# Kernel optimization log

Measured on AMD Instinct MI355X. Metric: run time of the kernel, lower is better.

## Reference

```python
import jax, jax.numpy as jnp
import numpy as np

SEQ_LEN, BATCH, VOCAB, EMB, HID, LAYERS = 70, 64, 10000, 512, 512, 2


def setup_inputs() -> dict:
    key = jax.random.key(0)
    ks = jax.random.split(key, 6)
    u = lambda k, shape: jax.random.uniform(k, shape, jnp.float32, -0.1, 0.1)
    return {
        "inputs": jax.random.randint(ks[0], (SEQ_LEN, BATCH), 0, VOCAB),  # token ids
        "hidden": jnp.zeros((LAYERS, BATCH, HID), jnp.float32),           # init_hidden()
        "emb_table": jax.random.normal(ks[1], (VOCAB, EMB), jnp.float32),  # nn.Embedding default N(0,1)
        "W0": u(ks[2], (HID, EMB + HID)),
        "b0": jnp.zeros((HID,), jnp.float32),
        "W1": u(ks[3], (HID, 2 * HID)),
        "b1": jnp.zeros((HID,), jnp.float32),
        "Wout": u(ks[4], (VOCAB, HID)),
        "bout": jnp.zeros((VOCAB,), jnp.float32),
    }


def reference(inputs, hidden, emb_table, W0, b0, W1, b1, Wout, bout):
    # Embedding lookup for whole sequence: (T, B, E)
    emb = emb_table[inputs]
    Ws, bs = [W0, W1], [b0, b1]

    def step(h, x_t):  # h: (L, B, H), x_t: (B, E)
        inp = x_t
        new_h = []
        for l in range(LAYERS):  # small fixed depth; layers are structurally distinct
            cat = jnp.concatenate([inp, h[l]], axis=1)          # (B, E+H) or (B, 2H)
            out = jnp.tanh(cat @ Ws[l].T + bs[l])               # (B, H)
            new_h.append(out)
            inp = out
        logits_t = jnp.tanh(inp @ Wout.T + bout)                # (B, V) (original applies Tanh to logits)
        return jnp.stack(new_h), logits_t

    h_final, logits = jax.lax.scan(step, hidden, emb)
    return logits, h_final
```

## Files before the change

### kernel.cpp

```cpp
#include <hip/hip_runtime.h>

#define T 70
#define B 64
#define E 512
#define H 512
#define V 10000
#define NP 10112
#define TB (T*B)
#define SLOT (H*B)
#define LOGITS_N (T*B*V)

#define WV_F 81920
#define WL_F 36864
#define WS_F4 35840
#define WLAYER 262144

typedef __attribute__((ext_vector_type(8))) short bh8;
typedef __attribute__((ext_vector_type(4))) float f32x4;

__device__ __forceinline__ float ftanh(float x) {
    float e = __expf(2.0f * x);
    return 1.0f - 2.0f / (e + 1.0f);
}

__device__ __forceinline__ unsigned short f2bf(float x) {
    unsigned int u = __float_as_uint(x);
    u += 0x7FFFu + ((u >> 16) & 1u);
    return (unsigned short)(u >> 16);
}
__device__ __forceinline__ float bf2f(unsigned short h) {
    return __uint_as_float(((unsigned int)h) << 16);
}

__global__ __launch_bounds__(256) void gather_emb(const int* __restrict__ ids,
                                                  const float* __restrict__ emb,
                                                  float* __restrict__ X) {
    int i = blockIdx.x * 256 + threadIdx.x;
    if (i >= TB * (E / 4)) return;
    int tok = i >> 7;
    int e4 = i & 127;
    int id = ids[tok];
    ((float4*)X)[i] = ((const float4*)emb)[id * 128 + e4];
}

__global__ __launch_bounds__(256) void pack_w(const float* __restrict__ W0,
                                              const float* __restrict__ W1,
                                              float* __restrict__ Wpk) {
    int g = blockIdx.x * 256 + threadIdx.x;
    int l = g >= 93184;
    int u = g - l * 93184;
    const float* S = l ? W1 : W0;
    float* D = Wpk + l * WLAYER;

    if (u < 20480) {
        int n2 = u & 255, q = u >> 8;
        int j2 = q % 40, hq = q / 40;
        int k = hq * 256 + 2 * j2;
        int n0 = 2 * n2;
        float2 r0 = *(const float2*)(S + (size_t)n0 * 1024 + 512 + k);
        float2 r1 = *(const float2*)(S + (size_t)(n0 + 1) * 1024 + 512 + k);
        ((float4*)D)[(hq * 40 + j2) * 256 + n2] = make_float4(r0.x, r1.x, r0.y, r1.y);
    } else if (u < 20480 + WS_F4) {
        int v = u - 20480;
        int n2 = v & 255, q = v >> 8;
        int j2s = q % 70, hq = q / 70;
        int k = hq * 256 + 116 + 2 * j2s;
        int n0 = 2 * n2;
        float2 r0 = *(const float2*)(S + (size_t)n0 * 1024 + 512 + k);
        float2 r1 = *(const float2*)(S + (size_t)(n0 + 1) * 1024 + 512 + k);
        ((float4*)D)[(WV_F + WL_F) / 4 + (hq * 70 + j2s) * 256 + n2] =
            make_float4(r0.x, r1.x, r0.y, r1.y);
    } else {
        int w = u - (20480 + WS_F4);
        int n = w & 511, q = w >> 9;
        int jr = q % 36, hq = q / 36;
        int k = hq * 256 + 80 + jr;
        D[WV_F + (hq * 36 + jr) * 512 + n] = S[(size_t)n * 1024 + 512 + k];
    }
}

__global__ __launch_bounds__(256) void split_w(const float* __restrict__ Wout,
                                               unsigned short* __restrict__ Whi,
                                               unsigned short* __restrict__ Wlo) {
    int i = blockIdx.x * 256 + threadIdx.x;
    if (i >= NP * 512) return;
    int v = i >> 9;
    float x = (v < V) ? Wout[i] : 0.f;
    unsigned short hi = f2bf(x);
    Whi[i] = hi;
    Wlo[i] = f2bf(x - bf2f(hi));
}

__global__ __launch_bounds__(256) void gemm_p0(const float* __restrict__ X,
                                               const float* __restrict__ W0,
                                               const float* __restrict__ b0v,
                                               float* __restrict__ P0) {
    __shared__ float As[32][68];
    __shared__ float Ws[32][68];
    int t = blockIdx.y;
    int n0 = blockIdx.x * 64;
    int tid = threadIdx.x;
    int bq = tid & 15;
    int nq = tid >> 4;
    const float* A = X + t * 64 * E;
    float acc[4][4] = {{0.f}};

    for (int kc = 0; kc < 512; kc += 32) {
        for (int i = tid; i < 512; i += 256) {
            int bb = i >> 3, kq = i & 7;
            float4 a = *(const float4*)(A + bb * E + kc + kq * 4);
            As[kq*4+0][bb] = a.x; As[kq*4+1][bb] = a.y;
            As[kq*4+2][bb] = a.z; As[kq*4+3][bb] = a.w;
        }
        for (int i = tid; i < 512; i += 256) {
            int nn = i >> 3, kq = i & 7;
            float4 w = *(const float4*)(W0 + (size_t)(n0 + nn) * 1024 + kc + kq * 4);
            Ws[kq*4+0][nn] = w.x; Ws[kq*4+1][nn] = w.y;
            Ws[kq*4+2][nn] = w.z; Ws[kq*4+3][nn] = w.w;
        }
        __syncthreads();
#pragma unroll
        for (int kk = 0; kk < 32; kk++) {
            float4 a = *(const float4*)&As[kk][bq * 4];
            float4 w = *(const float4*)&Ws[kk][nq * 4];
            acc[0][0] += a.x*w.x; acc[0][1] += a.x*w.y; acc[0][2] += a.x*w.z; acc[0][3] += a.x*w.w;
            acc[1][0] += a.y*w.x; acc[1][1] += a.y*w.y; acc[1][2] += a.y*w.z; acc[1][3] += a.y*w.w;
            acc[2][0] += a.z*w.x; acc[2][1] += a.z*w.y; acc[2][2] += a.z*w.z; acc[2][3] += a.z*w.w;
            acc[3][0] += a.w*w.x; acc[3][1] += a.w*w.y; acc[3][2] += a.w*w.z; acc[3][3] += a.w*w.w;
        }
        __syncthreads();
    }
    int nb = n0 + nq * 4;
    float4 bo = *(const float4*)(b0v + nb);
#pragma unroll
    for (int i = 0; i < 4; i++) {
        int bb = bq * 4 + i;
        float4 r = make_float4(acc[i][0] + bo.x, acc[i][1] + bo.y,
                               acc[i][2] + bo.z, acc[i][3] + bo.w);
        *(float4*)(P0 + (size_t)t * SLOT + bb * 512 + nb) = r;
    }
}

__global__ __launch_bounds__(256) void gemm_p1(const float* __restrict__ H0,
                                               const float* __restrict__ W1,
                                               const float* __restrict__ b1v,
                                               float* __restrict__ P1) {
    __shared__ float As[32][68];
    __shared__ float Ws[32][68];
    int t = blockIdx.y;
    int n0 = blockIdx.x * 64;
    int tid = threadIdx.x;
    int bq = tid & 15;
    int nq = tid >> 4;
    const float* A = H0 + (size_t)t * SLOT;
    float acc[4][4] = {{0.f}};

    for (int kc = 0; kc < 512; kc += 32) {
        for (int i = tid; i < 512; i += 256) {
            int bb = i >> 3, kq = i & 7;
            float4 a = *(const float4*)(A + bb * 512 + kc + kq * 4);
            As[kq*4+0][bb] = a.x; As[kq*4+1][bb] = a.y;
            As[kq*4+2][bb] = a.z; As[kq*4+3][bb] = a.w;
        }
        for (int i = tid; i < 512; i += 256) {
            int nn = i >> 3, kq = i & 7;
            float4 w = *(const float4*)(W1 + (size_t)(n0 + nn) * 1024 + kc + kq * 4);
            Ws[kq*4+0][nn] = w.x; Ws[kq*4+1][nn] = w.y;
            Ws[kq*4+2][nn] = w.z; Ws[kq*4+3][nn] = w.w;
        }
        __syncthreads();
#pragma unroll
        for (int kk = 0; kk < 32; kk++) {
            float4 a = *(const float4*)&As[kk][bq * 4];
            float4 w = *(const float4*)&Ws[kk][nq * 4];
            acc[0][0] += a.x*w.x; acc[0][1] += a.x*w.y; acc[0][2] += a.x*w.z; acc[0][3] += a.x*w.w;
            acc[1][0] += a.y*w.x; acc[1][1] += a.y*w.y; acc[1][2] += a.y*w.z; acc[1][3] += a.y*w.w;
            acc[2][0] += a.z*w.x; acc[2][1] += a.z*w.y; acc[2][2] += a.z*w.z; acc[2][3] += a.z*w.w;
            acc[3][0] += a.w*w.x; acc[3][1] += a.w*w.y; acc[3][2] += a.w*w.z; acc[3][3] += a.w*w.w;
        }
        __syncthreads();
    }
    int nb = n0 + nq * 4;
    float4 bo = *(const float4*)(b1v + nb);
#pragma unroll
    for (int i = 0; i < 4; i++) {
        int bb = bq * 4 + i;
        float4 r = make_float4(acc[i][0] + bo.x, acc[i][1] + bo.y,
                               acc[i][2] + bo.z, acc[i][3] + bo.w);
        *(float4*)(P1 + (size_t)t * SLOT + bb * 512 + nb) = r;
    }
}

#define RPT40(X) X(0) X(1) X(2) X(3) X(4) X(5) X(6) X(7) X(8) X(9) X(10) X(11) \
  X(12) X(13) X(14) X(15) X(16) X(17) X(18) X(19) X(20) X(21) X(22) X(23) \
  X(24) X(25) X(26) X(27) X(28) X(29) X(30) X(31) X(32) X(33) X(34) X(35) \
  X(36) X(37) X(38) X(39)
#define RPT20P(X) X(0,0,1) X(1,2,3) X(2,4,5) X(3,6,7) X(4,8,9) X(5,10,11) \
  X(6,12,13) X(7,14,15) X(8,16,17) X(9,18,19) X(10,20,21) X(11,22,23) \
  X(12,24,25) X(13,26,27) X(14,28,29) X(15,30,31) X(16,32,33) X(17,34,35) \
  X(18,36,37) X(19,38,39)

__global__ __launch_bounds__(512, 2) void chain_hyb(const float* __restrict__ P,
                                                    const float* __restrict__ hidden,
                                                    const float* __restrict__ Wp,
                                                    float* __restrict__ Hist,
                                                    unsigned short* __restrict__ Hhi,
                                                    unsigned short* __restrict__ Hlo,
                                                    float* __restrict__ out,
                                                    int layer) {
    __shared__ float lds_w[WL_F];
    __shared__ float hs[512];
    __shared__ float2 part2[256];
    int tid = threadIdx.x;
    int b   = blockIdx.x;
    int n2  = tid & 255;
    int hq  = tid >> 8;
    int n0  = 2 * n2;

    const float4* wv = (const float4*)Wp + hq * (40 * 256) + n2;
#define DECLW(i) float4 w##i = wv[(i) * 256];
    RPT40(DECLW)
#undef DECLW

    {
        const float4* wl4 = (const float4*)(Wp + WV_F);
        float4* l4 = (float4*)lds_w;
        for (int i = tid; i < WL_F / 4; i += 512) l4[i] = wl4[i];
    }
    hs[tid & 511] = hidden[layer * SLOT + b * 512 + (tid & 511)];

#define PINW(i) asm volatile("" : "+v"(w##i.x), "+v"(w##i.y), "+v"(w##i.z), "+v"(w##i.w));
    RPT40(PINW)
#undef PINW
    __syncthreads();

    const float4* wsp = (const float4*)(Wp + WV_F + WL_F) + hq * (70 * 256) + n2;
    const float4* hs4 = (const float4*)hs;
    const float2* ldsw2 = (const float2*)lds_w;
    int hql4 = hq * 64;
    int ksb  = hq * 256 + 116;

    for (int s = 0; s < T; s++) {
        float2 pin = make_float2(0.f, 0.f);
        if (hq == 0)
            pin = *(const float2*)(P + (size_t)s * SLOT + b * 512 + n0);

        float ax = 0.f, ay = 0.f;

#pragma unroll 8
        for (int j = 0; j < 70; j++) {
            float4 wv4 = wsp[j * 256];
            float2 h2 = *(const float2*)&hs[ksb + 2 * j];
            ax += wv4.x * h2.x + wv4.z * h2.y;
            ay += wv4.y * h2.x + wv4.w * h2.y;
        }

#define FMAV(m, A, B2) { float4 h4 = hs4[hql4 + (m)]; \
        ax += w##A.x * h4.x + w##A.z * h4.y + w##B2.x * h4.z + w##B2.z * h4.w; \
        ay += w##A.y * h4.x + w##A.w * h4.y + w##B2.y * h4.z + w##B2.w * h4.w; }
        RPT20P(FMAV)
#undef FMAV

#pragma unroll
        for (int g = 0; g < 9; g++) {
            float4 h4 = hs4[hql4 + 20 + g];
            float2 l0 = ldsw2[(hq * 36 + 4 * g + 0) * 256 + n2];
            float2 l1 = ldsw2[(hq * 36 + 4 * g + 1) * 256 + n2];
            float2 l2 = ldsw2[(hq * 36 + 4 * g + 2) * 256 + n2];
            float2 l3 = ldsw2[(hq * 36 + 4 * g + 3) * 256 + n2];
            ax += l0.x * h4.x + l1.x * h4.y + l2.x * h4.z + l3.x * h4.w;
            ay += l0.y * h4.x + l1.y * h4.y + l2.y * h4.z + l3.y * h4.w;
        }

        if (hq) part2[n2] = make_float2(ax, ay);
        __syncthreads();
        if (hq == 0) {
            float2 pr = part2[n2];
            float o0 = ftanh(pin.x + ax + pr.x);
            float o1 = ftanh(pin.y + ay + pr.y);
            hs[n0] = o0; hs[n0 + 1] = o1;
            if (layer == 0) {
                *(float2*)(Hist + (size_t)s * SLOT + b * 512 + n0) = make_float2(o0, o1);
            } else {
                size_t m = (size_t)(s * 64 + b) * 512 + n0;
                unsigned short h0 = f2bf(o0), h1 = f2bf(o1);
                Hhi[m] = h0;     Hhi[m + 1] = h1;
                Hlo[m] = f2bf(o0 - bf2f(h0));
                Hlo[m + 1] = f2bf(o1 - bf2f(h1));
            }
        }
        __syncthreads();
    }

    out[LOGITS_N + layer * SLOT + b * 512 + tid] = hs[tid];
}

__global__ __launch_bounds__(256, 2) void logits_mfma(const unsigned short* __restrict__ Ahi,
                                                      const unsigned short* __restrict__ Alo,
                                                      const unsigned short* __restrict__ Whi,
                                                      const unsigned short* __restrict__ Wlo,
                                                      const float* __restrict__ boutv,
                                                      float* __restrict__ out) {
    __shared__ unsigned short Ah[128 * 40], Al[128 * 40];
    __shared__ unsigned short Bh[128 * 40], Bl[128 * 40];
    int tid = threadIdx.x;
    int v0 = blockIdx.x * 128;
    int mb = blockIdx.y * 128;
    int lane = tid & 63;
    int wid = tid >> 6;
    int lr = lane & 15;
    int lg = lane >> 4;
    int mhalf = (wid & 1) * 64;
    int nhalf = (wid >> 1) * 64;

    f32x4 acc[4][4];
#pragma unroll
    for (int i = 0; i < 4; i++)
#pragma unroll
        for (int j = 0; j < 4; j++) {
            acc[i][j][0] = 0.f; acc[i][j][1] = 0.f;
            acc[i][j][2] = 0.f; acc[i][j][3] = 0.f;
        }

    int aoff[4], boff[4];
#pragma unroll
    for (int f = 0; f < 4; f++) {
        aoff[f] = (mhalf + f * 16 + lr) * 40 + lg * 8;
        boff[f] = (nhalf + f * 16 + lr) * 40 + lg * 8;
    }

    for (int kb = 0; kb < 512; kb += 32) {
#pragma unroll
        for (int it = 0; it < 2; ++it) {
            int idx = it * 256 + tid;
            int r = idx >> 2, u = idx & 3;
            int d = r * 40 + u * 8;
            size_t sA = (size_t)(mb + r) * 512 + kb + u * 8;
            size_t sB = (size_t)(v0 + r) * 512 + kb + u * 8;
            *(uint4*)&Ah[d] = *(const uint4*)&Ahi[sA];
            *(uint4*)&Al[d] = *(const uint4*)&Alo[sA];
            *(uint4*)&Bh[d] = *(const uint4*)&Whi[sB];
            *(uint4*)&Bl[d] = *(const uint4*)&Wlo[sB];
        }
        __syncthreads();

        bh8 ah[4], al[4], bh[4], bl[4];
#pragma unroll
        for (int f = 0; f < 4; f++) {
            ah[f] = *(const bh8*)&Ah[aoff[f]];
            al[f] = *(const bh8*)&Al[aoff[f]];
            bh[f] = *(const bh8*)&Bh[boff[f]];
            bl[f] = *(const bh8*)&Bl[boff[f]];
        }
#pragma unroll
        for (int mf = 0; mf < 4; mf++)
#pragma unroll
            for (int nf = 0; nf < 4; nf++) {
                acc[mf][nf] = __builtin_amdgcn_mfma_f32_16x16x32_bf16(ah[mf], bh[nf], acc[mf][nf], 0, 0, 0);
                acc[mf][nf] = __builtin_amdgcn_mfma_f32_16x16x32_bf16(ah[mf], bl[nf], acc[mf][nf], 0, 0, 0);
                acc[mf][nf] = __builtin_amdgcn_mfma_f32_16x16x32_bf16(al[mf], bh[nf], acc[mf][nf], 0, 0, 0);
            }
        __syncthreads();
    }

#pragma unroll
    for (int nf = 0; nf < 4; nf++) {
        int v = v0 + nhalf + nf * 16 + lr;
        if (v < V) {
            float bo = boutv[v];
#pragma unroll
            for (int mf = 0; mf < 4; mf++) {
                int gm = mb + mhalf + mf * 16 + lg * 4;
#pragma unroll
                for (int reg = 0; reg < 4; reg++)
                    out[(size_t)(gm + reg) * V + v] = ftanh(acc[mf][nf][reg] + bo);
            }
        }
    }
}

extern "C" void kernel_launch(void* const* d_in, const int* in_sizes, int n_in,
                              void* d_out, int out_size, void* d_ws, size_t ws_size,
                              hipStream_t stream) {
    const int*   ids    = (const int*)d_in[0];
    const float* hidden = (const float*)d_in[1];
    const float* emb    = (const float*)d_in[2];
    const float* W0     = (const float*)d_in[3];
    const float* b0v    = (const float*)d_in[4];
    const float* W1     = (const float*)d_in[5];
    const float* b1v    = (const float*)d_in[6];
    const float* Wout   = (const float*)d_in[7];
    const float* boutv  = (const float*)d_in[8];
    float* out = (float*)d_out;
    float* ws  = (float*)d_ws;

    float* X    = ws;
    float* P0   = ws + 2293760;
    float* H0   = ws + 4587520;
    float* Wpk  = ws + 6881280;
    float* P1   = X;
    unsigned short* H1hi = (unsigned short*)(ws + 2293760);
    unsigned short* H1lo = (unsigned short*)(ws + 2293760 + 1146880);
    unsigned short* Whi  = (unsigned short*)(ws + 7405568);
    unsigned short* Wlo  = (unsigned short*)(ws + 9994240);

    gather_emb<<<2240, 256, 0, stream>>>(ids, emb, X);
    pack_w<<<728, 256, 0, stream>>>(W0, W1, Wpk);
    split_w<<<(NP * 512) / 256, 256, 0, stream>>>(Wout, Whi, Wlo);
    gemm_p0<<<dim3(8, T), 256, 0, stream>>>(X, W0, b0v, P0);
    chain_hyb<<<64, 512, 0, stream>>>(P0, hidden, Wpk, H0, nullptr, nullptr, out, 0);
    gemm_p1<<<dim3(8, T), 256, 0, stream>>>(H0, W1, b1v, P1);
    chain_hyb<<<64, 512, 0, stream>>>(P1, hidden, Wpk + WLAYER, nullptr, H1hi, H1lo, out, 1);
    logits_mfma<<<dim3(NP / 128, TB / 128), 256, 0, stream>>>(H1hi, H1lo, Whi, Wlo, boutv, out);
}
```

Baseline: 1.337 ms.

## Rebalance recurrent weight split and enlarge logits MFMA tiles to 256x256

The recurrent chain kernel moves part of each layer's recurrent weights out of pinned registers (40 float4 down to 28) into a slightly larger LDS slice and a longer streamed-from-global slice. This lowers register pressure per thread, at the cost of more global/L2 traffic on every time step. The logits MFMA GEMM goes from 128x128 tiles with 256 threads to 256x256 tiles with 512 threads, giving more operand reuse per LDS load and fewer blocks. The larger tiles need bounds handling for rows and columns past the padded edges, and the last row tile reads some A data beyond the real sequence rows.

```diff
diff --git a/kernel.cpp b/kernel.cpp
--- a/kernel.cpp
+++ b/kernel.cpp
@@ -10,9 +10,9 @@
 #define SLOT (H*B)
 #define LOGITS_N (T*B*V)
 
-#define WV_F 81920
-#define WL_F 36864
-#define WS_F4 35840
+#define WV_F 57344
+#define WL_F 38912
+#define WS_F4 41472
 #define WLAYER 262144
 
 typedef __attribute__((ext_vector_type(8))) short bh8;
@@ -47,35 +47,35 @@
                                               const float* __restrict__ W1,
                                               float* __restrict__ Wpk) {
     int g = blockIdx.x * 256 + threadIdx.x;
-    int l = g >= 93184;
-    int u = g - l * 93184;
+    int l = g >= 94720;
+    int u = g - l * 94720;
     const float* S = l ? W1 : W0;
     float* D = Wpk + l * WLAYER;
 
-    if (u < 20480) {
+    if (u < 14336) {
         int n2 = u & 255, q = u >> 8;
-        int j2 = q % 40, hq = q / 40;
+        int j2 = q % 28, hq = q / 28;
         int k = hq * 256 + 2 * j2;
         int n0 = 2 * n2;
         float2 r0 = *(const float2*)(S + (size_t)n0 * 1024 + 512 + k);
         float2 r1 = *(const float2*)(S + (size_t)(n0 + 1) * 1024 + 512 + k);
-        ((float4*)D)[(hq * 40 + j2) * 256 + n2] = make_float4(r0.x, r1.x, r0.y, r1.y);
-    } else if (u < 20480 + WS_F4) {
-        int v = u - 20480;
+        ((float4*)D)[(hq * 28 + j2) * 256 + n2] = make_float4(r0.x, r1.x, r0.y, r1.y);
+    } else if (u < 14336 + WS_F4) {
+        int v = u - 14336;
         int n2 = v & 255, q = v >> 8;
-        int j2s = q % 70, hq = q / 70;
-        int k = hq * 256 + 116 + 2 * j2s;
+        int j2s = q % 81, hq = q / 81;
+        int k = hq * 256 + 94 + 2 * j2s;
         int n0 = 2 * n2;
         float2 r0 = *(const float2*)(S + (size_t)n0 * 1024 + 512 + k);
         float2 r1 = *(const float2*)(S + (size_t)(n0 + 1) * 1024 + 512 + k);
-        ((float4*)D)[(WV_F + WL_F) / 4 + (hq * 70 + j2s) * 256 + n2] =
+        ((float4*)D)[(WV_F + WL_F) / 4 + (hq * 81 + j2s) * 256 + n2] =
             make_float4(r0.x, r1.x, r0.y, r1.y);
     } else {
-        int w = u - (20480 + WS_F4);
+        int w = u - (14336 + WS_F4);
         int n = w & 511, q = w >> 9;
-        int jr = q % 36, hq = q / 36;
-        int k = hq * 256 + 80 + jr;
-        D[WV_F + (hq * 36 + jr) * 512 + n] = S[(size_t)n * 1024 + 512 + k];
+        int jr = q % 38, hq = q / 38;
+        int k = hq * 256 + 56 + jr;
+        D[WV_F + (hq * 38 + jr) * 512 + n] = S[(size_t)n * 1024 + 512 + k];
     }
 }
 
@@ -191,14 +191,12 @@
     }
 }
 
-#define RPT40(X) X(0) X(1) X(2) X(3) X(4) X(5) X(6) X(7) X(8) X(9) X(10) X(11) \
+#define RPT28(X) X(0) X(1) X(2) X(3) X(4) X(5) X(6) X(7) X(8) X(9) X(10) X(11) \
   X(12) X(13) X(14) X(15) X(16) X(17) X(18) X(19) X(20) X(21) X(22) X(23) \
-  X(24) X(25) X(26) X(27) X(28) X(29) X(30) X(31) X(32) X(33) X(34) X(35) \
-  X(36) X(37) X(38) X(39)
-#define RPT20P(X) X(0,0,1) X(1,2,3) X(2,4,5) X(3,6,7) X(4,8,9) X(5,10,11) \
+  X(24) X(25) X(26) X(27)
+#define RPT14P(X) X(0,0,1) X(1,2,3) X(2,4,5) X(3,6,7) X(4,8,9) X(5,10,11) \
   X(6,12,13) X(7,14,15) X(8,16,17) X(9,18,19) X(10,20,21) X(11,22,23) \
-  X(12,24,25) X(13,26,27) X(14,28,29) X(15,30,31) X(16,32,33) X(17,34,35) \
-  X(18,36,37) X(19,38,39)
+  X(12,24,25) X(13,26,27)
 
 __global__ __launch_bounds__(512, 2) void chain_hyb(const float* __restrict__ P,
                                                     const float* __restrict__ hidden,
@@ -217,9 +215,9 @@
     int hq  = tid >> 8;
     int n0  = 2 * n2;
 
-    const float4* wv = (const float4*)Wp + hq * (40 * 256) + n2;
+    const float4* wv = (const float4*)Wp + hq * (28 * 256) + n2;
 #define DECLW(i) float4 w##i = wv[(i) * 256];
-    RPT40(DECLW)
+    RPT28(DECLW)
 #undef DECLW
 
     {
@@ -230,15 +228,16 @@
     hs[tid & 511] = hidden[layer * SLOT + b * 512 + (tid & 511)];
 
 #define PINW(i) asm volatile("" : "+v"(w##i.x), "+v"(w##i.y), "+v"(w##i.z), "+v"(w##i.w));
-    RPT40(PINW)
+    RPT28(PINW)
 #undef PINW
     __syncthreads();
 
-    const float4* wsp = (const float4*)(Wp + WV_F + WL_F) + hq * (70 * 256) + n2;
+    const float4* wsp = (const float4*)(Wp + WV_F + WL_F) + hq * (81 * 256) + n2;
     const float4* hs4 = (const float4*)hs;
     const float2* ldsw2 = (const float2*)lds_w;
     int hql4 = hq * 64;
-    int ksb  = hq * 256 + 116;
+    int klb  = hq * 256 + 56;
+    int ksb  = hq * 256 + 94;
 
     for (int s = 0; s < T; s++) {
         float2 pin = make_float2(0.f, 0.f);
@@ -248,7 +247,7 @@
         float ax = 0.f, ay = 0.f;
 
 #pragma unroll 8
-        for (int j = 0; j < 70; j++) {
+        for (int j = 0; j < 81; j++) {
             float4 wv4 = wsp[j * 256];
             float2 h2 = *(const float2*)&hs[ksb + 2 * j];
             ax += wv4.x * h2.x + wv4.z * h2.y;
@@ -258,18 +257,16 @@
 #define FMAV(m, A, B2) { float4 h4 = hs4[hql4 + (m)]; \
         ax += w##A.x * h4.x + w##A.z * h4.y + w##B2.x * h4.z + w##B2.z * h4.w; \
         ay += w##A.y * h4.x + w##A.w * h4.y + w##B2.y * h4.z + w##B2.w * h4.w; }
-        RPT20P(FMAV)
+        RPT14P(FMAV)
 #undef FMAV
 
 #pragma unroll
-        for (int g = 0; g < 9; g++) {
-            float4 h4 = hs4[hql4 + 20 + g];
-            float2 l0 = ldsw2[(hq * 36 + 4 * g + 0) * 256 + n2];
-            float2 l1 = ldsw2[(hq * 36 + 4 * g + 1) * 256 + n2];
-            float2 l2 = ldsw2[(hq * 36 + 4 * g + 2) * 256 + n2];
-            float2 l3 = ldsw2[(hq * 36 + 4 * g + 3) * 256 + n2];
-            ax += l0.x * h4.x + l1.x * h4.y + l2.x * h4.z + l3.x * h4.w;
-            ay += l0.y * h4.x + l1.y * h4.y + l2.y * h4.z + l3.y * h4.w;
+        for (int g = 0; g < 19; g++) {
+            float2 h2 = *(const float2*)&hs[klb + 2 * g];
+            float2 l0 = ldsw2[(hq * 38 + 2 * g) * 256 + n2];
+            float2 l1 = ldsw2[(hq * 38 + 2 * g + 1) * 256 + n2];
+            ax += l0.x * h2.x + l1.x * h2.y;
+            ay += l0.y * h2.x + l1.y * h2.y;
         }
 
         if (hq) part2[n2] = make_float2(ax, ay);
@@ -295,85 +292,92 @@
     out[LOGITS_N + layer * SLOT + b * 512 + tid] = hs[tid];
 }
 
-__global__ __launch_bounds__(256, 2) void logits_mfma(const unsigned short* __restrict__ Ahi,
+__global__ __launch_bounds__(512, 2) void logits_mfma(const unsigned short* __restrict__ Ahi,
                                                       const unsigned short* __restrict__ Alo,
                                                       const unsigned short* __restrict__ Whi,
                                                       const unsigned short* __restrict__ Wlo,
                                                       const float* __restrict__ boutv,
                                                       float* __restrict__ out) {
-    __shared__ unsigned short Ah[128 * 40], Al[128 * 40];
-    __shared__ unsigned short Bh[128 * 40], Bl[128 * 40];
+    __shared__ unsigned short Ah[256 * 40], Al[256 * 40];
+    __shared__ unsigned short Bh[256 * 40], Bl[256 * 40];
     int tid = threadIdx.x;
-    int v0 = blockIdx.x * 128;
-    int mb = blockIdx.y * 128;
+    int v0 = blockIdx.x * 256;
+    int mb = blockIdx.y * 256;
     int lane = tid & 63;
     int wid = tid >> 6;
     int lr = lane & 15;
     int lg = lane >> 4;
-    int mhalf = (wid & 1) * 64;
-    int nhalf = (wid >> 1) * 64;
-
-    f32x4 acc[4][4];
-#pragma unroll
-    for (int i = 0; i < 4; i++)
+    int wm = wid & 1;
+    int wn = wid >> 1;
+
+    f32x4 acc[8][4];
+#pragma unroll
+    for (int i = 0; i < 8; i++)
 #pragma unroll
         for (int j = 0; j < 4; j++) {
             acc[i][j][0] = 0.f; acc[i][j][1] = 0.f;
             acc[i][j][2] = 0.f; acc[i][j][3] = 0.f;
         }
 
-    int aoff[4], boff[4];
-#pragma unroll
-    for (int f = 0; f < 4; f++) {
-        aoff[f] = (mhalf + f * 16 + lr) * 40 + lg * 8;
-        boff[f] = (nhalf + f * 16 + lr) * 40 + lg * 8;
-    }
+    int aoff[8], boff[4];
+#pragma unroll
+    for (int f = 0; f < 8; f++) aoff[f] = (wm * 128 + f * 16 + lr) * 40 + lg * 8;
+#pragma unroll
+    for (int f = 0; f < 4; f++) boff[f] = (wn * 64 + f * 16 + lr) * 40 + lg * 8;
+
+    const uint4 z4 = make_uint4(0u, 0u, 0u, 0u);
 
     for (int kb = 0; kb < 512; kb += 32) {
 #pragma unroll
         for (int it = 0; it < 2; ++it) {
-            int idx = it * 256 + tid;
+            int idx = it * 512 + tid;
             int r = idx >> 2, u = idx & 3;
             int d = r * 40 + u * 8;
             size_t sA = (size_t)(mb + r) * 512 + kb + u * 8;
-            size_t sB = (size_t)(v0 + r) * 512 + kb + u * 8;
             *(uint4*)&Ah[d] = *(const uint4*)&Ahi[sA];
             *(uint4*)&Al[d] = *(const uint4*)&Alo[sA];
-            *(uint4*)&Bh[d] = *(const uint4*)&Whi[sB];
-            *(uint4*)&Bl[d] = *(const uint4*)&Wlo[sB];
-        }
-        __syncthreads();
-
-        bh8 ah[4], al[4], bh[4], bl[4];
-#pragma unroll
-        for (int f = 0; f < 4; f++) {
-            ah[f] = *(const bh8*)&Ah[aoff[f]];
-            al[f] = *(const bh8*)&Al[aoff[f]];
-            bh[f] = *(const bh8*)&Bh[boff[f]];
-            bl[f] = *(const bh8*)&Bl[boff[f]];
-        }
-#pragma unroll
-        for (int mf = 0; mf < 4; mf++)
+            int rB = v0 + r;
+            size_t sB = (size_t)rB * 512 + kb + u * 8;
+            bool okB = rB < NP;
+            *(uint4*)&Bh[d] = okB ? *(const uint4*)&Whi[sB] : z4;
+            *(uint4*)&Bl[d] = okB ? *(const uint4*)&Wlo[sB] : z4;
+        }
+        __syncthreads();
+
+        bh8 bhf[4], blf[4];
+#pragma unroll
+        for (int nf = 0; nf < 4; nf++) {
+            bhf[nf] = *(const bh8*)&Bh[boff[nf]];
+            blf[nf] = *(const bh8*)&Bl[boff[nf]];
+        }
+#pragma unroll
+        for (int mf = 0; mf < 8; mf++) {
+            bh8 ah = *(const bh8*)&Ah[aoff[mf]];
+            bh8 al = *(const bh8*)&Al[aoff[mf]];
 #pragma unroll
             for (int nf = 0; nf < 4; nf++) {
-                acc[mf][nf] = __builtin_amdgcn_mfma_f32_16x16x32_bf16(ah[mf], bh[nf], acc[mf][nf], 0, 0, 0);
-                acc[mf][nf] = __builtin_amdgcn_mfma_f32_16x16x32_bf16(ah[mf], bl[nf], acc[mf][nf], 0, 0, 0);
-                acc[mf][nf] = __builtin_amdgcn_mfma_f32_16x16x32_bf16(al[mf], bh[nf], acc[mf][nf], 0, 0, 0);
+                acc[mf][nf] = __builtin_amdgcn_mfma_f32_16x16x32_bf16(ah, bhf[nf], acc[mf][nf], 0, 0, 0);
+                acc[mf][nf] = __builtin_amdgcn_mfma_f32_16x16x32_bf16(ah, blf[nf], acc[mf][nf], 0, 0, 0);
+                acc[mf][nf] = __builtin_amdgcn_mfma_f32_16x16x32_bf16(al, bhf[nf], acc[mf][nf], 0, 0, 0);
             }
+        }
         __syncthreads();
     }
 
 #pragma unroll
     for (int nf = 0; nf < 4; nf++) {
-        int v = v0 + nhalf + nf * 16 + lr;
+        int v = v0 + wn * 64 + nf * 16 + lr;
         if (v < V) {
             float bo = boutv[v];
 #pragma unroll
-            for (int mf = 0; mf < 4; mf++) {
-                int gm = mb + mhalf + mf * 16 + lg * 4;
-#pragma unroll
-                for (int reg = 0; reg < 4; reg++)
-                    out[(size_t)(gm + reg) * V + v] = ftanh(acc[mf][nf][reg] + bo);
+            for (int mf = 0; mf < 8; mf++) {
+                int gmb = mb + wm * 128 + mf * 16;
+                if (gmb < TB) {
+                    int gm = gmb + lg * 4;
+#pragma unroll
+                    for (int reg = 0; reg < 4; reg++)
+                        out[(size_t)(gm + reg) * V + v] = ftanh(acc[mf][nf][reg] + bo);
+                }
             }
         }
     }
@@ -405,11 +409,11 @@
     unsigned short* Wlo  = (unsigned short*)(ws + 9994240);
 
     gather_emb<<<2240, 256, 0, stream>>>(ids, emb, X);
-    pack_w<<<728, 256, 0, stream>>>(W0, W1, Wpk);
+    pack_w<<<740, 256, 0, stream>>>(W0, W1, Wpk);
     split_w<<<(NP * 512) / 256, 256, 0, stream>>>(Wout, Whi, Wlo);
     gemm_p0<<<dim3(8, T), 256, 0, stream>>>(X, W0, b0v, P0);
     chain_hyb<<<64, 512, 0, stream>>>(P0, hidden, Wpk, H0, nullptr, nullptr, out, 0);
     gemm_p1<<<dim3(8, T), 256, 0, stream>>>(H0, W1, b1v, P1);
     chain_hyb<<<64, 512, 0, stream>>>(P1, hidden, Wpk + WLAYER, nullptr, H1hi, H1lo, out, 1);
-    logits_mfma<<<dim3(NP / 128, TB / 128), 256, 0, stream>>>(H1hi, H1lo, Whi, Wlo, boutv, out);
-}
+    logits_mfma<<<dim3((NP + 255) / 256, (TB + 255) / 256), 512, 0, stream>>>(H1hi, H1lo, Whi, Wlo, boutv, out);
+}
```

After: 1.429 ms. 6.9% more time.
